# Kernel tuning notes

Measured on AMD Instinct MI355X. Metric: run time of the kernel, lower is better.

Reference implementation:

```python
import jax, jax.numpy as jnp
import numpy as np

N = 50000      # n_nodes
E = 800000     # n_edges
IN_NF = 64     # in_node_nf
HID = 128      # hidden_nf
OUT_NF = 64    # out_node_nf
L = 4          # n_layers
EH = HID // 2  # edge MLP hidden width (edge_nf_ratio=2)
C = 1.0        # aggregation scaling constant


def _w(k, shape):
    # fan-in scaled init (matches nn.Linear scale roughly)
    return jax.random.normal(k, shape, dtype=jnp.float32) / np.sqrt(shape[-2]).astype(np.float32)


def setup_inputs() -> dict:
    key = jax.random.key(0)
    ks = jax.random.split(key, 10)
    h = jax.random.normal(ks[0], (N, IN_NF), dtype=jnp.float32)
    edges = jax.random.randint(ks[1], (2, E), 0, N, dtype=jnp.int32)
    return {
        "h": h,
        "edges": edges,
        "W_in": _w(ks[2], (IN_NF, HID)),
        "b_in": jnp.zeros((HID,), jnp.float32),
        # stacked per-layer GCL params, leading dim L
        "eW1": _w(ks[3], (L, 2 * HID, EH)),
        "eb1": jnp.zeros((L, EH), jnp.float32),
        "eW2": _w(ks[4], (L, EH, EH)),
        "eb2": jnp.zeros((L, EH), jnp.float32),
        "nW1": _w(ks[5], (L, HID + EH, HID)),
        "nb1": jnp.zeros((L, HID), jnp.float32),
        "nW2": _w(ks[6], (L, HID, HID)),
        "nb2": jnp.zeros((L, HID), jnp.float32),
        "W_out": _w(ks[7], (HID, OUT_NF)),
        "b_out": jnp.zeros((OUT_NF,), jnp.float32),
    }


def reference(h, edges, W_in, b_in, eW1, eb1, eW2, eb2, nW1, nb1, nW2, nb2, W_out, b_out):
    row, col = edges[0], edges[1]
    h = h @ W_in + b_in  # [N, HID] embedding_in

    def layer(hc, p):
        w1, b1, w2, b2, m1, c1, m2, c2 = p
        # edge model: gather endpoints, concat, 2-layer SiLU MLP
        m = jnp.concatenate([hc[row], hc[col]], axis=1)          # [E, 2*HID]
        m = jax.nn.silu(m @ w1 + b1)                             # [E, EH]
        m = jax.nn.silu(m @ w2 + b2)                             # [E, EH]
        # node model: scatter-sum messages to source nodes, scale by C
        agg = jax.ops.segment_sum(m, row, num_segments=N) * C    # [N, EH]
        z = jnp.concatenate([hc, agg], axis=1)                   # [N, HID+EH]
        z = jax.nn.silu(z @ m1 + c1)
        z = z @ m2 + c2                                          # [N, HID]
        return hc + z, None  # residual=True

    h, _ = jax.lax.scan(layer, h, (eW1, eb1, eW2, eb2, nW1, nb1, nW2, nb2))
    return h @ W_out + b_out  # [N, OUT_NF] embedding_out
```

## Files before the change

### kernel.cpp

```cpp
#include <hip/hip_runtime.h>
#include <hip/hip_bf16.h>
#include <hip/hip_fp16.h>
#include <cstdint>
#include <cstddef>

#define N_NODES 50000
#define N_EDGES 800000
#define NBKT    196
#define BSH     8
#define BCHUNK  2048
#define CAP     6144

typedef __attribute__((ext_vector_type(8))) short short8;
typedef __attribute__((ext_vector_type(4))) float floatx4;
typedef __attribute__((ext_vector_type(2))) float floatx2;
typedef __attribute__((ext_vector_type(4))) unsigned int uintx4;
typedef __attribute__((ext_vector_type(2))) unsigned int uintx2;
typedef __attribute__((ext_vector_type(8))) _Float16 half8v;

__device__ inline float bf2f(unsigned short u) {
    union { unsigned int i; float f; } v; v.i = ((unsigned int)u) << 16; return v.f;
}
__device__ inline unsigned short f2bf(float f) {
    union { float f; unsigned int i; } v; v.f = f;
    unsigned int u = v.i;
    return (unsigned short)((u + 0x7FFFu + ((u >> 16) & 1u)) >> 16);
}
__device__ inline unsigned int f2bf_pk(float a, float b) {
    __hip_bfloat162 h2 = __float22bfloat162_rn(make_float2(a, b));
    return *reinterpret_cast<unsigned int*>(&h2);
}
__device__ inline unsigned short f2fh(float f) {
    _Float16 h = (_Float16)f;
    return __builtin_bit_cast(unsigned short, h);
}
__device__ inline unsigned int f2fh_pk(float a, float b) {
    typedef __attribute__((ext_vector_type(2))) __fp16 h2v;
    h2v r = __builtin_amdgcn_cvt_pkrtz(a, b);
    return __builtin_bit_cast(unsigned int, r);
}
__device__ inline __half2 u2h(unsigned int u) { return __builtin_bit_cast(__half2, u); }
__device__ inline unsigned int h2u(__half2 h) { return __builtin_bit_cast(unsigned int, h); }
__device__ inline __half2 silu_h2(__half2 x) {
    const __half2 nlog2e = __float2half2_rn(-1.4426950408889634f);
    const __half2 one    = __float2half2_rn(1.0f);
    __half2 e = h2exp2(__hmul2(x, nlog2e));
    return __hmul2(x, h2rcp(__hadd2(e, one)));
}
__device__ inline float silu_f(float x) {
    float e = __expf(-x);
    return x * __builtin_amdgcn_rcpf(1.0f + e);
}

__device__ inline int block_excl_scan_256(int v, int* buf) {
    int tid = threadIdx.x;
    buf[tid] = v;
    __syncthreads();
    #pragma unroll
    for (int off = 1; off < 256; off <<= 1) {
        int t = (tid >= off) ? buf[tid - off] : 0;
        __syncthreads();
        buf[tid] += t;
        __syncthreads();
    }
    return buf[tid] - v;
}

__device__ inline void pack_std(const float* __restrict__ src,
                                unsigned short* __restrict__ dst,
                                int NOUT, long j) {
    int i = (int)(j & 7);
    long rest = j >> 3;
    int n = (int)(rest % NOUT);
    int kb = (int)(rest / NOUT);
    dst[j] = f2bf(src[(long)(kb * 8 + i) * NOUT + n]);
}
__device__ inline void pack_std_h(const float* __restrict__ src,
                                  unsigned short* __restrict__ dst,
                                  int NOUT, long j) {
    int i = (int)(j & 7);
    long rest = j >> 3;
    int n = (int)(rest % NOUT);
    int kb = (int)(rest / NOUT);
    dst[j] = f2fh(src[(long)(kb * 8 + i) * NOUT + n]);
}

#define SW_IN 8192L
#define SW_OUT 8192L
#define SW1   16384L
#define SE2   4096L
#define SN1   24576L
#define SN2   16384L
#define SB    128L
#define PERL  (SW1 + SE2 + SN1 + SN2 + SB)
#define PACK_TOTAL (SW_IN + SW_OUT + 4 * PERL)
#define PACK_GRID_TOTAL (PACK_TOTAL + NBKT)

__global__ __launch_bounds__(256) void pack_kernel(
    const float* __restrict__ W_in,
    const float* __restrict__ W_out, const float* __restrict__ eW1,
    const float* __restrict__ eb1, const float* __restrict__ eW2,
    const float* __restrict__ nW1, const float* __restrict__ nW2,
    unsigned short* __restrict__ Winp,
    unsigned short* __restrict__ Woutp, unsigned short* __restrict__ W1p,
    unsigned short* __restrict__ eW2p, unsigned short* __restrict__ nW1p,
    unsigned short* __restrict__ nW2p, float* __restrict__ biasP,
    int* __restrict__ countB)
{
    long idx = (long)blockIdx.x * 256 + threadIdx.x;
    if (idx >= PACK_TOTAL) {
        long t = idx - PACK_TOTAL;
        if (t < NBKT) countB[t] = 0;
        return;
    }
    long j = idx;
    if (j < SW_IN) { pack_std(W_in, Winp, 128, j); return; }
    j -= SW_IN;
    if (j < SW_OUT) { pack_std(W_out, Woutp, 64, j); return; }
    j -= SW_OUT;
    int l = (int)(j / PERL);
    long r = j % PERL;
    if (r < SW1) {
        int i = (int)(r & 7);
        int n = (int)((r >> 3) & 127);
        int kb = (int)(r >> 10);
        int k = kb * 8 + i;
        const float* w = eW1 + (long)l * 256 * 64;
        float v = (n < 64) ? w[(long)k * 64 + n] : w[(long)(128 + k) * 64 + (n - 64)];
        W1p[(long)l * SW1 + r] = f2bf(v);
        return;
    }
    r -= SW1;
    if (r < SE2) { pack_std_h(eW2 + (long)l * 4096, eW2p + (long)l * SE2, 64, r); return; }
    r -= SE2;
    if (r < SN1) { pack_std(nW1 + (long)l * 24576, nW1p + (long)l * SN1, 128, r); return; }
    r -= SN1;
    if (r < SN2) { pack_std(nW2 + (long)l * 16384, nW2p + (long)l * SN2, 128, r); return; }
    r -= SN2;
    biasP[(long)l * 128 + r] = (r < 64) ? eb1[(long)l * 64 + r] : 0.0f;
}

__global__ __launch_bounds__(256) void hist_k(const int* __restrict__ erow,
                                              int* __restrict__ countB, int E) {
    __shared__ int c[NBKT];
    for (int i = threadIdx.x; i < NBKT; i += 256) c[i] = 0;
    __syncthreads();
    int j = blockIdx.x * BCHUNK + threadIdx.x;
    #pragma unroll
    for (int i = 0; i < BCHUNK / 256; i++, j += 256)
        if (j < E) atomicAdd(&c[erow[j] >> BSH], 1);
    __syncthreads();
    for (int i = threadIdx.x; i < NBKT; i += 256)
        if (c[i]) atomicAdd(&countB[i], c[i]);
}

__global__ __launch_bounds__(256) void bucket_scan_k(const int* __restrict__ countB,
                                                     int* __restrict__ bucketBase,
                                                     int* __restrict__ bucketCursor) {
    __shared__ int buf[256];
    int tid = threadIdx.x;
    int v = (tid < NBKT) ? countB[tid] : 0;
    int excl = block_excl_scan_256(v, buf);
    if (tid < NBKT) {
        bucketBase[tid] = excl;
        bucketCursor[tid] = excl;
    }
    if (tid == NBKT - 1) bucketBase[NBKT] = excl + v;
}

__global__ __launch_bounds__(256) void bin_k(
    const int* __restrict__ erow, const int* __restrict__ ecol,
    int* __restrict__ bucketCursor, int2* __restrict__ binned, int E)
{
    __shared__ int2 staged[BCHUNK];
    __shared__ int cnt[NBKT];
    __shared__ int binStart[NBKT];
    __shared__ int gbase[NBKT];
    __shared__ int scanbuf[256];
    const int tid = threadIdx.x;
    const int base = blockIdx.x * BCHUNK;
    const int nloc = min(BCHUNK, E - base);

    for (int i = tid; i < NBKT; i += 256) cnt[i] = 0;
    __syncthreads();

    int2 ed[BCHUNK / 256];
    int  bo[BCHUNK / 256];
    #pragma unroll
    for (int i = 0; i < BCHUNK / 256; i++) {
        int jl = i * 256 + tid;
        if (jl < nloc) {
            int j = base + jl;
            int r = erow[j], c = ecol[j];
            ed[i] = make_int2(r, c);
            int b = r >> BSH;
            int off = atomicAdd(&cnt[b], 1);
            bo[i] = (b << 12) | off;
        } else bo[i] = -1;
    }
    __syncthreads();

    int v = (tid < NBKT) ? cnt[tid] : 0;
    int excl = block_excl_scan_256(v, scanbuf);
    if (tid < NBKT) binStart[tid] = excl;
    if (tid < NBKT && v > 0) gbase[tid] = atomicAdd(&bucketCursor[tid], v);
    __syncthreads();

    #pragma unroll
    for (int i = 0; i < BCHUNK / 256; i++) {
        if (bo[i] >= 0)
            staged[binStart[bo[i] >> 12] + (bo[i] & 0xFFF)] = ed[i];
    }
    __syncthreads();

    for (int j = tid; j < nloc; j += 256) {
        int2 e = staged[j];
        int b = e.x >> BSH;
        binned[gbase[b] + (j - binStart[b])] = e;
    }
}

__global__ __launch_bounds__(256) void sort_k(
    const int2* __restrict__ binned, const int* __restrict__ bucketBase,
    int2* __restrict__ eidx)
{
    __shared__ int2 st[CAP];
    __shared__ int cnt[256];
    __shared__ int cur[256];
    __shared__ int scanbuf[256];
    const int b = blockIdx.x;
    const int tid = threadIdx.x;
    const int s0 = bucketBase[b];
    int n = bucketBase[b + 1] - s0;
    if (n > CAP) n = CAP;

    cnt[tid] = 0;
    __syncthreads();
    for (int j = tid; j < n; j += 256) {
        int2 e = binned[s0 + j];
        st[j] = e;
        atomicAdd(&cnt[e.x & 255], 1);
    }
    __syncthreads();
    int excl = block_excl_scan_256(cnt[tid], scanbuf);
    cur[tid] = excl;
    __syncthreads();
    for (int j = tid; j < n; j += 256) {
        int2 e = st[j];
        int pos = atomicAdd(&cur[e.x & 255], 1);
        eidx[s0 + pos] = e;
    }
}

__global__ __launch_bounds__(256) void edge_fused_k(
    const int2* __restrict__ eidx,
    const unsigned short* __restrict__ P,
    const unsigned short* __restrict__ Bp,
    const float* __restrict__ b2, float* __restrict__ agg, int E)
{
    __shared__ float M2s[64 * 68];
    __shared__ int ridS[64];
    __shared__ short segStartS[66];
    __shared__ int nsegS;
    const int tid = threadIdx.x;
    const int wave = tid >> 6;
    const int lane = tid & 63;
    const int lrow = lane & 15;
    const int quad = lane >> 4;
    const int e0 = blockIdx.x * 64;
    const int el = wave * 16 + lrow;
    const int e = e0 + el;

    floatx4 acc[4];
    #pragma unroll
    for (int nt = 0; nt < 4; nt++) {
        float bv = b2[nt * 16 + lrow];
        acc[nt] = (floatx4){bv, bv, bv, bv};
    }

    half8v af0 = {};
    half8v af1 = {};
    if (e < E) {
        int2 rc = eidx[e];
        int rr = rc.x, cc = rc.y;
        if (quad == 0) ridS[el] = rr;
        const uintx4* pt = (const uintx4*)(P + (size_t)rr * 128 + quad * 8);
        const uintx4* pb = (const uintx4*)(P + (size_t)cc * 128 + 64 + quad * 8);
        uintx4 t0 = pt[0], t1 = pt[4];
        uintx4 b0 = pb[0], b1 = pb[4];
        uintx4 O0, O1;
        #pragma unroll
        for (int i = 0; i < 4; i++) {
            O0[i] = h2u(silu_h2(__hadd2(u2h(t0[i]), u2h(b0[i]))));
            O1[i] = h2u(silu_h2(__hadd2(u2h(t1[i]), u2h(b1[i]))));
        }
        af0 = __builtin_bit_cast(half8v, O0);
        af1 = __builtin_bit_cast(half8v, O1);
    } else if (quad == 0) {
        ridS[el] = -1;
    }

    #pragma unroll
    for (int nt = 0; nt < 4; nt++) {
        half8v bf0 = *(const half8v*)(Bp + (size_t)((0 * 4 + quad) * 64 + nt * 16 + lrow) * 8);
        acc[nt] = __builtin_amdgcn_mfma_f32_16x16x32_f16(af0, bf0, acc[nt], 0, 0, 0);
        half8v bf1 = *(const half8v*)(Bp + (size_t)((1 * 4 + quad) * 64 + nt * 16 + lrow) * 8);
        acc[nt] = __builtin_amdgcn_mfma_f32_16x16x32_f16(af1, bf1, acc[nt], 0, 0, 0);
    }

    #pragma unroll
    for (int nt = 0; nt < 4; nt++) {
        int n = nt * 16 + lrow;
        #pragma unroll
        for (int r = 0; r < 4; r++) {
            int el2 = wave * 16 + quad * 4 + r;
            M2s[el2 * 68 + n] = silu_f(acc[nt][r]);
        }
    }
    __syncthreads();

    if (tid < 64) {
        bool st = (ridS[tid] >= 0) && (tid == 0 || ridS[tid] != ridS[tid - 1]);
        unsigned long long m = __ballot(st);
        if (st) {
            int pos = __popcll(m & ((1ull << tid) - 1));
            segStartS[pos] = (short)tid;
        }
        if (tid == 0) {
            int ns = __popcll(m);
            nsegS = ns;
            int nvalid = E - e0;
            if (nvalid > 64) nvalid = 64;
            segStartS[ns] = (short)nvalid;
        }
    }
    __syncthreads();

    {
        int f = tid & 63;
        int g = tid >> 6;
        int ns = nsegS;
        for (int j = g; j < ns; j += 4) {
            int a = segStartS[j], b = segStartS[j + 1];
            float s = 0.0f;
            for (int el2 = a; el2 < b; el2++) s += M2s[el2 * 68 + f];
            int rv = ridS[a];
            if (j == 0 || j == ns - 1)
                atomicAdd(&agg[(size_t)rv * 64 + f], s);
            else
                agg[(size_t)rv * 64 + f] = s;
        }
    }
}

#define SROW 264
template<int FINAL>
__global__ __launch_bounds__(512) void node_fused_k(
    const unsigned short* __restrict__ hbf, const float* __restrict__ agg,
    const unsigned short* __restrict__ W1, const float* __restrict__ b1,
    const unsigned short* __restrict__ W2, const float* __restrict__ b2,
    const unsigned short* __restrict__ B3, const float* __restrict__ bias3,
    unsigned short* __restrict__ hB, unsigned short* __restrict__ Pout,
    float* __restrict__ outF, float* __restrict__ aggZ, int M)
{
    __shared__ unsigned short S[64 * SROW];
    const int tid = threadIdx.x;
    const int m0 = blockIdx.x * 64;
    const int wave = tid >> 6;
    const int lane = tid & 63;
    const int lrow = lane & 15;
    const int quad = lane >> 4;
    const int g = wave >> 1;
    const int h = wave & 1;
    const int elb = g * 16 + quad * 4;

    short8 afa0, afa1;
    {
        const float* ap = agg + (size_t)(m0 + g * 16 + lrow) * 64;
        floatx4 q0 = *(const floatx4*)(ap + quad * 8);
        floatx4 q1 = *(const floatx4*)(ap + quad * 8 + 4);
        floatx4 q2 = *(const floatx4*)(ap + 32 + quad * 8);
        floatx4 q3 = *(const floatx4*)(ap + 32 + quad * 8 + 4);
        unsigned int c0[4] = { f2bf_pk(q0[0], q0[1]), f2bf_pk(q0[2], q0[3]),
                               f2bf_pk(q1[0], q1[1]), f2bf_pk(q1[2], q1[3]) };
        unsigned int c1[4] = { f2bf_pk(q2[0], q2[1]), f2bf_pk(q2[2], q2[3]),
                               f2bf_pk(q3[0], q3[1]), f2bf_pk(q3[2], q3[3]) };
        afa0 = *(const short8*)c0;
        afa1 = *(const short8*)c1;
    }

    for (int t = tid; t < 64 * 16; t += 512) {
        int rr = t >> 4, c = t & 15;
        int row = m0 + rr;
        uintx4 val = {0, 0, 0, 0};
        if (row < M) val = *(const uintx4*)(hbf + (size_t)row * 128 + c * 8);
        *(uintx4*)(&S[rr * SROW + c * 8]) = val;
    }
    __syncthreads();

    if (!FINAL) {
        floatx4 z = {0, 0, 0, 0};
        for (int t = tid; t < 64 * 16; t += 512) {
            int rr = t >> 4, c = t & 15;
            int row = m0 + rr;
            if (row < M) *(floatx4*)(aggZ + (size_t)row * 64 + c * 4) = z;
        }
    }

    const unsigned short* arow = &S[(g * 16 + lrow) * SROW];

    floatx4 acc[4];
    #pragma unroll
    for (int i = 0; i < 4; i++) acc[i] = (floatx4){0, 0, 0, 0};
    #pragma unroll
    for (int kt = 0; kt < 4; kt++) {
        short8 afrag = *(const short8*)(arow + kt * 32 + quad * 8);
        int kb = kt * 4 + quad;
        #pragma unroll
        for (int j = 0; j < 4; j++) {
            int n = (4 * h + j) * 16 + lrow;
            short8 bfrag = *(const short8*)(W1 + (size_t)(kb * 128 + n) * 8);
            acc[j] = __builtin_amdgcn_mfma_f32_16x16x32_bf16(afrag, bfrag, acc[j], 0, 0, 0);
        }
    }
    #pragma unroll
    for (int j = 0; j < 4; j++) {
        int n = (4 * h + j) * 16 + lrow;
        short8 b4 = *(const short8*)(W1 + (size_t)((16 + quad) * 128 + n) * 8);
        acc[j] = __builtin_amdgcn_mfma_f32_16x16x32_bf16(afa0, b4, acc[j], 0, 0, 0);
        short8 b5 = *(const short8*)(W1 + (size_t)((20 + quad) * 128 + n) * 8);
        acc[j] = __builtin_amdgcn_mfma_f32_16x16x32_bf16(afa1, b5, acc[j], 0, 0, 0);
    }

    #pragma unroll
    for (int j = 0; j < 4; j++) {
        int n = (4 * h + j) * 16 + lrow;
        float bv = b1[n];
        unsigned int p01 = f2bf_pk(silu_f(acc[j][0] + bv), silu_f(acc[j][1] + bv));
        unsigned int p23 = f2bf_pk(silu_f(acc[j][2] + bv), silu_f(acc[j][3] + bv));
        S[(elb + 0) * SROW + 128 + n] = (unsigned short)(p01 & 0xFFFF);
        S[(elb + 1) * SROW + 128 + n] = (unsigned short)(p01 >> 16);
        S[(elb + 2) * SROW + 128 + n] = (unsigned short)(p23 & 0xFFFF);
        S[(elb + 3) * SROW + 128 + n] = (unsigned short)(p23 >> 16);
    }
    __syncthreads();

    floatx4 acc2[4];
    #pragma unroll
    for (int i = 0; i < 4; i++) acc2[i] = (floatx4){0, 0, 0, 0};
    #pragma unroll
    for (int kt = 0; kt < 4; kt++) {
        short8 afrag = *(const short8*)(arow + 128 + kt * 32 + quad * 8);
        int kb = kt * 4 + quad;
        #pragma unroll
        for (int j = 0; j < 4; j++) {
            int n = (4 * h + j) * 16 + lrow;
            short8 bfrag = *(const short8*)(W2 + (size_t)(kb * 128 + n) * 8);
            acc2[j] = __builtin_amdgcn_mfma_f32_16x16x32_bf16(afrag, bfrag, acc2[j], 0, 0, 0);
        }
    }

    #pragma unroll
    for (int j = 0; j < 4; j++) {
        int n = (4 * h + j) * 16 + lrow;
        float bv = b2[n];
        floatx4 v4;
        #pragma unroll
        for (int r = 0; r < 4; r++) {
            float res = bf2f(S[(elb + r) * SROW + n]);
            v4[r] = acc2[j][r] + bv + res;
        }
        unsigned int p01 = f2bf_pk(v4[0], v4[1]);
        unsigned int p23 = f2bf_pk(v4[2], v4[3]);
        S[(elb + 0) * SROW + n] = (unsigned short)(p01 & 0xFFFF);
        S[(elb + 1) * SROW + n] = (unsigned short)(p01 >> 16);
        S[(elb + 2) * SROW + n] = (unsigned short)(p23 & 0xFFFF);
        S[(elb + 3) * SROW + n] = (unsigned short)(p23 >> 16);
    }
    __syncthreads();

    constexpr int NT3 = FINAL ? 2 : 4;
    constexpr int NO3 = FINAL ? 64 : 128;
    floatx4 acc3[NT3];
    #pragma unroll
    for (int i = 0; i < NT3; i++) acc3[i] = (floatx4){0, 0, 0, 0};
    #pragma unroll
    for (int kt = 0; kt < 4; kt++) {
        short8 afrag = *(const short8*)(arow + kt * 32 + quad * 8);
        int kb = kt * 4 + quad;
        #pragma unroll
        for (int j = 0; j < NT3; j++) {
            int n = (NT3 * h + j) * 16 + lrow;
            short8 bfrag = *(const short8*)(B3 + (size_t)(kb * NO3 + n) * 8);
            acc3[j] = __builtin_amdgcn_mfma_f32_16x16x32_bf16(afrag, bfrag, acc3[j], 0, 0, 0);
        }
    }
    #pragma unroll
    for (int j = 0; j < NT3; j++) {
        int n = (NT3 * h + j) * 16 + lrow;
        float bv = bias3[n];
        if (FINAL) {
            #pragma unroll
            for (int r = 0; r < 4; r++)
                ((float*)(&S[(elb + r) * SROW + 128]))[n] = acc3[j][r] + bv;
        } else {
            unsigned int p01 = f2fh_pk(acc3[j][0] + bv, acc3[j][1] + bv);
            unsigned int p23 = f2fh_pk(acc3[j][2] + bv, acc3[j][3] + bv);
            S[(elb + 0) * SROW + 128 + n] = (unsigned short)(p01 & 0xFFFF);
            S[(elb + 1) * SROW + 128 + n] = (unsigned short)(p01 >> 16);
            S[(elb + 2) * SROW + 128 + n] = (unsigned short)(p23 & 0xFFFF);
            S[(elb + 3) * SROW + 128 + n] = (unsigned short)(p23 >> 16);
        }
    }
    __syncthreads();

    if (FINAL) {
        for (int t = tid; t < 64 * 16; t += 512) {
            int rr = t >> 4, c = t & 15;
            int row = m0 + rr;
            if (row < M)
                *(floatx4*)(outF + (size_t)row * 64 + c * 4) =
                    *(const floatx4*)((const float*)(&S[rr * SROW + 128]) + c * 4);
        }
    } else {
        for (int t = tid; t < 64 * 32; t += 512) {
            int rr = t >> 5, c = t & 31;
            int row = m0 + rr;
            if (row < M) {
                if (c < 16)
                    *(uintx4*)(hB + (size_t)row * 128 + c * 8) =
                        *(const uintx4*)(&S[rr * SROW + c * 8]);
                else
                    *(uintx4*)(Pout + (size_t)row * 128 + (c - 16) * 8) =
                        *(const uintx4*)(&S[rr * SROW + 128 + (c - 16) * 8]);
            }
        }
    }
}

#define SROWE 264
__global__ __launch_bounds__(256) void embed_fused_k(
    const float* __restrict__ h0, const unsigned short* __restrict__ Win,
    const float* __restrict__ b_in, const unsigned short* __restrict__ W1,
    const float* __restrict__ biasP,
    unsigned short* __restrict__ hB, unsigned short* __restrict__ Pout,
    float* __restrict__ aggZ, int M)
{
    __shared__ unsigned short S[64 * SROWE];
    const int tid = threadIdx.x;
    const int m0 = blockIdx.x * 64;
    const int wave = tid >> 6;
    const int lane = tid & 63;
    const int lrow = lane & 15;
    const int quad = lane >> 4;
    const int elb = wave * 16 + quad * 4;

    for (int t = tid; t < 64 * 16; t += 256) {
        int rr = t >> 4, c = t & 15;
        int row = m0 + rr;
        floatx4 v = {0, 0, 0, 0};
        if (row < M) v = *(const floatx4*)(h0 + (size_t)row * 64 + c * 4);
        uintx2 u = { f2bf_pk(v[0], v[1]), f2bf_pk(v[2], v[3]) };
        *(uintx2*)(&S[rr * SROWE + c * 4]) = u;
    }
    __syncthreads();

    {
        floatx4 z = {0, 0, 0, 0};
        for (int t = tid; t < 64 * 16; t += 256) {
            int rr = t >> 4, c = t & 15;
            int row = m0 + rr;
            if (row < M) *(floatx4*)(aggZ + (size_t)row * 64 + c * 4) = z;
        }
    }

    const unsigned short* arow = &S[(wave * 16 + lrow) * SROWE];

    floatx4 acc[8];
    #pragma unroll
    for (int i = 0; i < 8; i++) acc[i] = (floatx4){0, 0, 0, 0};
    #pragma unroll
    for (int kt = 0; kt < 2; kt++) {
        short8 afrag = *(const short8*)(arow + kt * 32 + quad * 8);
        int kb = kt * 4 + quad;
        #pragma unroll
        for (int nt = 0; nt < 8; nt++) {
            short8 bfrag = *(const short8*)(Win + (size_t)(kb * 128 + nt * 16 + lrow) * 8);
            acc[nt] = __builtin_amdgcn_mfma_f32_16x16x32_bf16(afrag, bfrag, acc[nt], 0, 0, 0);
        }
    }

    #pragma unroll
    for (int nt = 0; nt < 8; nt++) {
        int n = nt * 16 + lrow;
        float bv = b_in[n];
        floatx4 v4;
        #pragma unroll
        for (int r = 0; r < 4; r++) v4[r] = acc[nt][r] + bv;
        unsigned int p01 = f2bf_pk(v4[0], v4[1]);
        unsigned int p23 = f2bf_pk(v4[2], v4[3]);
        S[(elb + 0) * SROWE + n] = (unsigned short)(p01 & 0xFFFF);
        S[(elb + 1) * SROWE + n] = (unsigned short)(p01 >> 16);
        S[(elb + 2) * SROWE + n] = (unsigned short)(p23 & 0xFFFF);
        S[(elb + 3) * SROWE + n] = (unsigned short)(p23 >> 16);
    }

    floatx4 acc3[8];
    #pragma unroll
    for (int i = 0; i < 8; i++) acc3[i] = (floatx4){0, 0, 0, 0};
    #pragma unroll
    for (int kt = 0; kt < 4; kt++) {
        short8 afrag = *(const short8*)(arow + kt * 32 + quad * 8);
        int kb = kt * 4 + quad;
        #pragma unroll
        for (int nt = 0; nt < 8; nt++) {
            short8 bfrag = *(const short8*)(W1 + (size_t)(kb * 128 + nt * 16 + lrow) * 8);
            acc3[nt] = __builtin_amdgcn_mfma_f32_16x16x32_bf16(afrag, bfrag, acc3[nt], 0, 0, 0);
        }
    }
    #pragma unroll
    for (int nt = 0; nt < 8; nt++) {
        int n = nt * 16 + lrow;
        float bv = biasP[n];
        unsigned int p01 = f2fh_pk(acc3[nt][0] + bv, acc3[nt][1] + bv);
        unsigned int p23 = f2fh_pk(acc3[nt][2] + bv, acc3[nt][3] + bv);
        S[(elb + 0) * SROWE + 128 + n] = (unsigned short)(p01 & 0xFFFF);
        S[(elb + 1) * SROWE + 128 + n] = (unsigned short)(p01 >> 16);
        S[(elb + 2) * SROWE + 128 + n] = (unsigned short)(p23 & 0xFFFF);
        S[(elb + 3) * SROWE + 128 + n] = (unsigned short)(p23 >> 16);
    }
    __syncthreads();

    for (int t = tid; t < 64 * 32; t += 256) {
        int rr = t / 32, c = t % 32;
        int row = m0 + rr;
        if (row < M) {
            if (c < 16)
                *(uintx4*)(hB + (size_t)row * 128 + c * 8) =
                    *(const uintx4*)(&S[rr * SROWE + c * 8]);
            else
                *(uintx4*)(Pout + (size_t)row * 128 + (c - 16) * 8) =
                    *(const uintx4*)(&S[rr * SROWE + 128 + (c - 16) * 8]);
        }
    }
}

extern "C" void kernel_launch(void* const* d_in, const int* in_sizes, int n_in,
                              void* d_out, int out_size, void* d_ws, size_t ws_size,
                              hipStream_t stream) {
    const float* h0   = (const float*)d_in[0];
    const int*   edges= (const int*)d_in[1];
    const float* W_in = (const float*)d_in[2];
    const float* b_in = (const float*)d_in[3];
    const float* eW1  = (const float*)d_in[4];
    const float* eb1  = (const float*)d_in[5];
    const float* eW2  = (const float*)d_in[6];
    const float* eb2  = (const float*)d_in[7];
    const float* nW1  = (const float*)d_in[8];
    const float* nb1  = (const float*)d_in[9];
    const float* nW2  = (const float*)d_in[10];
    const float* nb2  = (const float*)d_in[11];
    const float* W_out= (const float*)d_in[12];
    const float* b_out= (const float*)d_in[13];
    float* out = (float*)d_out;

    const int E = in_sizes[1] / 2;
    const int* erow = edges;
    const int* ecol = edges + E;

    char* ws = (char*)d_ws;
    unsigned short* hbf  = (unsigned short*)(ws + 0);
    unsigned short* P    = (unsigned short*)(ws + 38424576);
    float*          agg  = (float*)(ws + 51224576);
    int2*           binned=(int2*)(ws + 51224576);
    int2*           eidx = (int2*)(ws + 76824576);
    float*          biasP= (float*)(ws + 83224576);
    unsigned short* Winp = (unsigned short*)(ws + 83226624);
    unsigned short* Woutp= (unsigned short*)(ws + 83243008);
    unsigned short* W1p  = (unsigned short*)(ws + 83259392);
    unsigned short* eW2p = (unsigned short*)(ws + 83390464);
    unsigned short* nW1p = (unsigned short*)(ws + 83423232);
    unsigned short* nW2p = (unsigned short*)(ws + 83619840);
    int*            countB=(int*)(ws + 83750912);
    int*            bucketBase=(int*)(ws + 83751936);
    int*            bucketCursor=(int*)(ws + 83752960);

    const int gemm_grid = (N_NODES + 63) / 64;
    const int edge_grid = (E + 63) / 64;
    const int pack_grid = (int)((PACK_GRID_TOTAL + 255) / 256);
    const int bin_grid  = (E + BCHUNK - 1) / BCHUNK;

    pack_kernel<<<pack_grid, 256, 0, stream>>>(W_in, W_out, eW1, eb1, eW2,
                                               nW1, nW2, Winp, Woutp, W1p,
                                               eW2p, nW1p, nW2p, biasP, countB);

    hist_k<<<bin_grid, 256, 0, stream>>>(erow, countB, E);
    bucket_scan_k<<<1, 256, 0, stream>>>(countB, bucketBase, bucketCursor);
    bin_k<<<bin_grid, 256, 0, stream>>>(erow, ecol, bucketCursor, binned, E);
    sort_k<<<NBKT, 256, 0, stream>>>(binned, bucketBase, eidx);

    embed_fused_k<<<gemm_grid, 256, 0, stream>>>(
        h0, Winp, b_in, W1p, biasP, hbf, P, agg, N_NODES);

    for (int l = 0; l < 4; l++) {
        edge_fused_k<<<edge_grid, 256, 0, stream>>>(
            eidx, P, eW2p + (size_t)l * SE2, eb2 + (size_t)l * 64, agg, E);
        if (l < 3) {
            node_fused_k<0><<<gemm_grid, 512, 0, stream>>>(
                hbf, agg, nW1p + (size_t)l * SN1, nb1 + (size_t)l * 128,
                nW2p + (size_t)l * SN2, nb2 + (size_t)l * 128,
                W1p + (size_t)(l + 1) * SW1, biasP + (size_t)(l + 1) * 128,
                hbf, P, nullptr, agg, N_NODES);
        } else {
            node_fused_k<1><<<gemm_grid, 512, 0, stream>>>(
                hbf, agg, nW1p + (size_t)l * SN1, nb1 + (size_t)l * 128,
                nW2p + (size_t)l * SN2, nb2 + (size_t)l * 128,
                Woutp, b_out, nullptr, nullptr, out, nullptr, N_NODES);
        }
    }
}
```

Measured before the change: 401.1 us.

## Merge bucket scan and embedding into binning kernel to cut launches

Drops the single-block bucket scan kernel. Each binning block and each sort block now recomputes the 196-entry exclusive scan of bucket counts, and cursors start at zero in the pack kernel. The binning work and the embedding GEMM run as different block ranges of one launch, so they can overlap and two launches are saved. The binned buffer moves to its own workspace region so it no longer overlaps agg, which the embedding blocks zero in the same launch.

```diff
diff --git a/kernel.cpp b/kernel.cpp
--- a/kernel.cpp
+++ b/kernel.cpp
@@ -94,7 +94,7 @@
 #define SB    128L
 #define PERL  (SW1 + SE2 + SN1 + SN2 + SB)
 #define PACK_TOTAL (SW_IN + SW_OUT + 4 * PERL)
-#define PACK_GRID_TOTAL (PACK_TOTAL + NBKT)
+#define PACK_GRID_TOTAL (PACK_TOTAL + 2 * NBKT)
 
 __global__ __launch_bounds__(256) void pack_kernel(
     const float* __restrict__ W_in,
@@ -105,12 +105,13 @@
     unsigned short* __restrict__ Woutp, unsigned short* __restrict__ W1p,
     unsigned short* __restrict__ eW2p, unsigned short* __restrict__ nW1p,
     unsigned short* __restrict__ nW2p, float* __restrict__ biasP,
-    int* __restrict__ countB)
+    int* __restrict__ countB, int* __restrict__ bucketCursor)
 {
     long idx = (long)blockIdx.x * 256 + threadIdx.x;
     if (idx >= PACK_TOTAL) {
         long t = idx - PACK_TOTAL;
         if (t < NBKT) countB[t] = 0;
+        else if (t < 2 * NBKT) bucketCursor[t - NBKT] = 0;
         return;
     }
     long j = idx;
@@ -154,84 +155,194 @@
         if (c[i]) atomicAdd(&countB[i], c[i]);
 }
 
-__global__ __launch_bounds__(256) void bucket_scan_k(const int* __restrict__ countB,
-                                                     int* __restrict__ bucketBase,
-                                                     int* __restrict__ bucketCursor) {
-    __shared__ int buf[256];
-    int tid = threadIdx.x;
-    int v = (tid < NBKT) ? countB[tid] : 0;
-    int excl = block_excl_scan_256(v, buf);
-    if (tid < NBKT) {
-        bucketBase[tid] = excl;
-        bucketCursor[tid] = excl;
-    }
-    if (tid == NBKT - 1) bucketBase[NBKT] = excl + v;
-}
-
-__global__ __launch_bounds__(256) void bin_k(
+#define SROWE 264
+#define BE_SMEM_BYTES (64 * SROWE * 2)
+
+__global__ __launch_bounds__(256) void bin_embed_k(
     const int* __restrict__ erow, const int* __restrict__ ecol,
-    int* __restrict__ bucketCursor, int2* __restrict__ binned, int E)
+    const int* __restrict__ countB, int* __restrict__ bucketCursor,
+    int2* __restrict__ binned, int E, int binGrid,
+    const float* __restrict__ h0, const unsigned short* __restrict__ Win,
+    const float* __restrict__ b_in, const unsigned short* __restrict__ W1,
+    const float* __restrict__ biasP,
+    unsigned short* __restrict__ hB, unsigned short* __restrict__ Pout,
+    float* __restrict__ aggZ, int M)
 {
-    __shared__ int2 staged[BCHUNK];
-    __shared__ int cnt[NBKT];
-    __shared__ int binStart[NBKT];
-    __shared__ int gbase[NBKT];
-    __shared__ int scanbuf[256];
+    __shared__ char SMEM[BE_SMEM_BYTES];
     const int tid = threadIdx.x;
-    const int base = blockIdx.x * BCHUNK;
-    const int nloc = min(BCHUNK, E - base);
-
-    for (int i = tid; i < NBKT; i += 256) cnt[i] = 0;
-    __syncthreads();
-
-    int2 ed[BCHUNK / 256];
-    int  bo[BCHUNK / 256];
-    #pragma unroll
-    for (int i = 0; i < BCHUNK / 256; i++) {
-        int jl = i * 256 + tid;
-        if (jl < nloc) {
-            int j = base + jl;
-            int r = erow[j], c = ecol[j];
-            ed[i] = make_int2(r, c);
-            int b = r >> BSH;
-            int off = atomicAdd(&cnt[b], 1);
-            bo[i] = (b << 12) | off;
-        } else bo[i] = -1;
-    }
-    __syncthreads();
-
-    int v = (tid < NBKT) ? cnt[tid] : 0;
-    int excl = block_excl_scan_256(v, scanbuf);
-    if (tid < NBKT) binStart[tid] = excl;
-    if (tid < NBKT && v > 0) gbase[tid] = atomicAdd(&bucketCursor[tid], v);
-    __syncthreads();
-
-    #pragma unroll
-    for (int i = 0; i < BCHUNK / 256; i++) {
-        if (bo[i] >= 0)
-            staged[binStart[bo[i] >> 12] + (bo[i] & 0xFFF)] = ed[i];
-    }
-    __syncthreads();
-
-    for (int j = tid; j < nloc; j += 256) {
-        int2 e = staged[j];
-        int b = e.x >> BSH;
-        binned[gbase[b] + (j - binStart[b])] = e;
+
+    if (blockIdx.x < binGrid) {
+        int* cnt      = (int*)SMEM;
+        int* binStart = cnt + NBKT;
+        int* gbase    = binStart + NBKT;
+        int* scanbuf  = gbase + NBKT;
+        int2* staged  = (int2*)(scanbuf + 256);
+
+        const int base = blockIdx.x * BCHUNK;
+        const int nloc = min(BCHUNK, E - base);
+
+        int vcb = (tid < NBKT) ? countB[tid] : 0;
+        int exclB = block_excl_scan_256(vcb, scanbuf);
+
+        for (int i = tid; i < NBKT; i += 256) cnt[i] = 0;
+        __syncthreads();
+
+        int2 ed[BCHUNK / 256];
+        int  bo[BCHUNK / 256];
+        #pragma unroll
+        for (int i = 0; i < BCHUNK / 256; i++) {
+            int jl = i * 256 + tid;
+            if (jl < nloc) {
+                int j = base + jl;
+                int r = erow[j], c = ecol[j];
+                ed[i] = make_int2(r, c);
+                int b = r >> BSH;
+                int off = atomicAdd(&cnt[b], 1);
+                bo[i] = (b << 12) | off;
+            } else bo[i] = -1;
+        }
+        __syncthreads();
+
+        int v = (tid < NBKT) ? cnt[tid] : 0;
+        int excl = block_excl_scan_256(v, scanbuf);
+        if (tid < NBKT) binStart[tid] = excl;
+        if (tid < NBKT && v > 0)
+            gbase[tid] = exclB + atomicAdd(&bucketCursor[tid], v);
+        __syncthreads();
+
+        #pragma unroll
+        for (int i = 0; i < BCHUNK / 256; i++) {
+            if (bo[i] >= 0)
+                staged[binStart[bo[i] >> 12] + (bo[i] & 0xFFF)] = ed[i];
+        }
+        __syncthreads();
+
+        for (int j = tid; j < nloc; j += 256) {
+            int2 e = staged[j];
+            int b = e.x >> BSH;
+            binned[gbase[b] + (j - binStart[b])] = e;
+        }
+        return;
+    }
+
+    unsigned short* S = (unsigned short*)SMEM;
+    const int m0 = (blockIdx.x - binGrid) * 64;
+    const int wave = tid >> 6;
+    const int lane = tid & 63;
+    const int lrow = lane & 15;
+    const int quad = lane >> 4;
+    const int elb = wave * 16 + quad * 4;
+
+    for (int t = tid; t < 64 * 16; t += 256) {
+        int rr = t >> 4, c = t & 15;
+        int row = m0 + rr;
+        floatx4 v = {0, 0, 0, 0};
+        if (row < M) v = *(const floatx4*)(h0 + (size_t)row * 64 + c * 4);
+        uintx2 u = { f2bf_pk(v[0], v[1]), f2bf_pk(v[2], v[3]) };
+        *(uintx2*)(&S[rr * SROWE + c * 4]) = u;
+    }
+    __syncthreads();
+
+    {
+        floatx4 z = {0, 0, 0, 0};
+        for (int t = tid; t < 64 * 16; t += 256) {
+            int rr = t >> 4, c = t & 15;
+            int row = m0 + rr;
+            if (row < M) *(floatx4*)(aggZ + (size_t)row * 64 + c * 4) = z;
+        }
+    }
+
+    const unsigned short* arow = &S[(wave * 16 + lrow) * SROWE];
+
+    floatx4 acc[8];
+    #pragma unroll
+    for (int i = 0; i < 8; i++) acc[i] = (floatx4){0, 0, 0, 0};
+    #pragma unroll
+    for (int kt = 0; kt < 2; kt++) {
+        short8 afrag = *(const short8*)(arow + kt * 32 + quad * 8);
+        int kb = kt * 4 + quad;
+        #pragma unroll
+        for (int nt = 0; nt < 8; nt++) {
+            short8 bfrag = *(const short8*)(Win + (size_t)(kb * 128 + nt * 16 + lrow) * 8);
+            acc[nt] = __builtin_amdgcn_mfma_f32_16x16x32_bf16(afrag, bfrag, acc[nt], 0, 0, 0);
+        }
+    }
+
+    #pragma unroll
+    for (int nt = 0; nt < 8; nt++) {
+        int n = nt * 16 + lrow;
+        float bv = b_in[n];
+        floatx4 v4;
+        #pragma unroll
+        for (int r = 0; r < 4; r++) v4[r] = acc[nt][r] + bv;
+        unsigned int p01 = f2bf_pk(v4[0], v4[1]);
+        unsigned int p23 = f2bf_pk(v4[2], v4[3]);
+        S[(elb + 0) * SROWE + n] = (unsigned short)(p01 & 0xFFFF);
+        S[(elb + 1) * SROWE + n] = (unsigned short)(p01 >> 16);
+        S[(elb + 2) * SROWE + n] = (unsigned short)(p23 & 0xFFFF);
+        S[(elb + 3) * SROWE + n] = (unsigned short)(p23 >> 16);
+    }
+
+    floatx4 acc3[8];
+    #pragma unroll
+    for (int i = 0; i < 8; i++) acc3[i] = (floatx4){0, 0, 0, 0};
+    #pragma unroll
+    for (int kt = 0; kt < 4; kt++) {
+        short8 afrag = *(const short8*)(arow + kt * 32 + quad * 8);
+        int kb = kt * 4 + quad;
+        #pragma unroll
+        for (int nt = 0; nt < 8; nt++) {
+            short8 bfrag = *(const short8*)(W1 + (size_t)(kb * 128 + nt * 16 + lrow) * 8);
+            acc3[nt] = __builtin_amdgcn_mfma_f32_16x16x32_bf16(afrag, bfrag, acc3[nt], 0, 0, 0);
+        }
+    }
+    #pragma unroll
+    for (int nt = 0; nt < 8; nt++) {
+        int n = nt * 16 + lrow;
+        float bv = biasP[n];
+        unsigned int p01 = f2fh_pk(acc3[nt][0] + bv, acc3[nt][1] + bv);
+        unsigned int p23 = f2fh_pk(acc3[nt][2] + bv, acc3[nt][3] + bv);
+        S[(elb + 0) * SROWE + 128 + n] = (unsigned short)(p01 & 0xFFFF);
+        S[(elb + 1) * SROWE + 128 + n] = (unsigned short)(p01 >> 16);
+        S[(elb + 2) * SROWE + 128 + n] = (unsigned short)(p23 & 0xFFFF);
+        S[(elb + 3) * SROWE + 128 + n] = (unsigned short)(p23 >> 16);
+    }
+    __syncthreads();
+
+    for (int t = tid; t < 64 * 32; t += 256) {
+        int rr = t / 32, c = t % 32;
+        int row = m0 + rr;
+        if (row < M) {
+            if (c < 16)
+                *(uintx4*)(hB + (size_t)row * 128 + c * 8) =
+                    *(const uintx4*)(&S[rr * SROWE + c * 8]);
+            else
+                *(uintx4*)(Pout + (size_t)row * 128 + (c - 16) * 8) =
+                    *(const uintx4*)(&S[rr * SROWE + 128 + (c - 16) * 8]);
+        }
     }
 }
 
 __global__ __launch_bounds__(256) void sort_k(
-    const int2* __restrict__ binned, const int* __restrict__ bucketBase,
+    const int2* __restrict__ binned, const int* __restrict__ countB,
     int2* __restrict__ eidx)
 {
     __shared__ int2 st[CAP];
     __shared__ int cnt[256];
     __shared__ int cur[256];
     __shared__ int scanbuf[256];
+    __shared__ int baseS[2];
     const int b = blockIdx.x;
     const int tid = threadIdx.x;
-    const int s0 = bucketBase[b];
-    int n = bucketBase[b + 1] - s0;
+
+    {
+        int v = (tid < NBKT) ? countB[tid] : 0;
+        int excl = block_excl_scan_256(v, scanbuf);
+        if (tid == b) { baseS[0] = excl; baseS[1] = excl + v; }
+    }
+    __syncthreads();
+    const int s0 = baseS[0];
+    int n = baseS[1] - s0;
     if (n > CAP) n = CAP;
 
     cnt[tid] = 0;
@@ -538,113 +649,6 @@
     }
 }
 
-#define SROWE 264
-__global__ __launch_bounds__(256) void embed_fused_k(
-    const float* __restrict__ h0, const unsigned short* __restrict__ Win,
-    const float* __restrict__ b_in, const unsigned short* __restrict__ W1,
-    const float* __restrict__ biasP,
-    unsigned short* __restrict__ hB, unsigned short* __restrict__ Pout,
-    float* __restrict__ aggZ, int M)
-{
-    __shared__ unsigned short S[64 * SROWE];
-    const int tid = threadIdx.x;
-    const int m0 = blockIdx.x * 64;
-    const int wave = tid >> 6;
-    const int lane = tid & 63;
-    const int lrow = lane & 15;
-    const int quad = lane >> 4;
-    const int elb = wave * 16 + quad * 4;
-
-    for (int t = tid; t < 64 * 16; t += 256) {
-        int rr = t >> 4, c = t & 15;
-        int row = m0 + rr;
-        floatx4 v = {0, 0, 0, 0};
-        if (row < M) v = *(const floatx4*)(h0 + (size_t)row * 64 + c * 4);
-        uintx2 u = { f2bf_pk(v[0], v[1]), f2bf_pk(v[2], v[3]) };
-        *(uintx2*)(&S[rr * SROWE + c * 4]) = u;
-    }
-    __syncthreads();
-
-    {
-        floatx4 z = {0, 0, 0, 0};
-        for (int t = tid; t < 64 * 16; t += 256) {
-            int rr = t >> 4, c = t & 15;
-            int row = m0 + rr;
-            if (row < M) *(floatx4*)(aggZ + (size_t)row * 64 + c * 4) = z;
-        }
-    }
-
-    const unsigned short* arow = &S[(wave * 16 + lrow) * SROWE];
-
-    floatx4 acc[8];
-    #pragma unroll
-    for (int i = 0; i < 8; i++) acc[i] = (floatx4){0, 0, 0, 0};
-    #pragma unroll
-    for (int kt = 0; kt < 2; kt++) {
-        short8 afrag = *(const short8*)(arow + kt * 32 + quad * 8);
-        int kb = kt * 4 + quad;
-        #pragma unroll
-        for (int nt = 0; nt < 8; nt++) {
-            short8 bfrag = *(const short8*)(Win + (size_t)(kb * 128 + nt * 16 + lrow) * 8);
-            acc[nt] = __builtin_amdgcn_mfma_f32_16x16x32_bf16(afrag, bfrag, acc[nt], 0, 0, 0);
-        }
-    }
-
-    #pragma unroll
-    for (int nt = 0; nt < 8; nt++) {
-        int n = nt * 16 + lrow;
-        float bv = b_in[n];
-        floatx4 v4;
-        #pragma unroll
-        for (int r = 0; r < 4; r++) v4[r] = acc[nt][r] + bv;
-        unsigned int p01 = f2bf_pk(v4[0], v4[1]);
-        unsigned int p23 = f2bf_pk(v4[2], v4[3]);
-        S[(elb + 0) * SROWE + n] = (unsigned short)(p01 & 0xFFFF);
-        S[(elb + 1) * SROWE + n] = (unsigned short)(p01 >> 16);
-        S[(elb + 2) * SROWE + n] = (unsigned short)(p23 & 0xFFFF);
-        S[(elb + 3) * SROWE + n] = (unsigned short)(p23 >> 16);
-    }
-
-    floatx4 acc3[8];
-    #pragma unroll
-    for (int i = 0; i < 8; i++) acc3[i] = (floatx4){0, 0, 0, 0};
-    #pragma unroll
-    for (int kt = 0; kt < 4; kt++) {
-        short8 afrag = *(const short8*)(arow + kt * 32 + quad * 8);
-        int kb = kt * 4 + quad;
-        #pragma unroll
-        for (int nt = 0; nt < 8; nt++) {
-            short8 bfrag = *(const short8*)(W1 + (size_t)(kb * 128 + nt * 16 + lrow) * 8);
-            acc3[nt] = __builtin_amdgcn_mfma_f32_16x16x32_bf16(afrag, bfrag, acc3[nt], 0, 0, 0);
-        }
-    }
-    #pragma unroll
-    for (int nt = 0; nt < 8; nt++) {
-        int n = nt * 16 + lrow;
-        float bv = biasP[n];
-        unsigned int p01 = f2fh_pk(acc3[nt][0] + bv, acc3[nt][1] + bv);
-        unsigned int p23 = f2fh_pk(acc3[nt][2] + bv, acc3[nt][3] + bv);
-        S[(elb + 0) * SROWE + 128 + n] = (unsigned short)(p01 & 0xFFFF);
-        S[(elb + 1) * SROWE + 128 + n] = (unsigned short)(p01 >> 16);
-        S[(elb + 2) * SROWE + 128 + n] = (unsigned short)(p23 & 0xFFFF);
-        S[(elb + 3) * SROWE + 128 + n] = (unsigned short)(p23 >> 16);
-    }
-    __syncthreads();
-
-    for (int t = tid; t < 64 * 32; t += 256) {
-        int rr = t / 32, c = t % 32;
-        int row = m0 + rr;
-        if (row < M) {
-            if (c < 16)
-                *(uintx4*)(hB + (size_t)row * 128 + c * 8) =
-                    *(const uintx4*)(&S[rr * SROWE + c * 8]);
-            else
-                *(uintx4*)(Pout + (size_t)row * 128 + (c - 16) * 8) =
-                    *(const uintx4*)(&S[rr * SROWE + 128 + (c - 16) * 8]);
-        }
-    }
-}
-
 extern "C" void kernel_launch(void* const* d_in, const int* in_sizes, int n_in,
                               void* d_out, int out_size, void* d_ws, size_t ws_size,
                               hipStream_t stream) {
@@ -670,9 +674,9 @@
 
     char* ws = (char*)d_ws;
     unsigned short* hbf  = (unsigned short*)(ws + 0);
+    int2*           binned=(int2*)(ws + 12800000);
     unsigned short* P    = (unsigned short*)(ws + 38424576);
     float*          agg  = (float*)(ws + 51224576);
-    int2*           binned=(int2*)(ws + 51224576);
     int2*           eidx = (int2*)(ws + 76824576);
     float*          biasP= (float*)(ws + 83224576);
     unsigned short* Winp = (unsigned short*)(ws + 83226624);
@@ -682,7 +686,6 @@
     unsigned short* nW1p = (unsigned short*)(ws + 83423232);
     unsigned short* nW2p = (unsigned short*)(ws + 83619840);
     int*            countB=(int*)(ws + 83750912);
-    int*            bucketBase=(int*)(ws + 83751936);
     int*            bucketCursor=(int*)(ws + 83752960);
 
     const int gemm_grid = (N_NODES + 63) / 64;
@@ -692,15 +695,16 @@
 
     pack_kernel<<<pack_grid, 256, 0, stream>>>(W_in, W_out, eW1, eb1, eW2,
                                                nW1, nW2, Winp, Woutp, W1p,
-                                               eW2p, nW1p, nW2p, biasP, countB);
+                                               eW2p, nW1p, nW2p, biasP,
+                                               countB, bucketCursor);
 
     hist_k<<<bin_grid, 256, 0, stream>>>(erow, countB, E);
-    bucket_scan_k<<<1, 256, 0, stream>>>(countB, bucketBase, bucketCursor);
-    bin_k<<<bin_grid, 256, 0, stream>>>(erow, ecol, bucketCursor, binned, E);
-    sort_k<<<NBKT, 256, 0, stream>>>(binned, bucketBase, eidx);
-
-    embed_fused_k<<<gemm_grid, 256, 0, stream>>>(
+
+    bin_embed_k<<<bin_grid + gemm_grid, 256, 0, stream>>>(
+        erow, ecol, countB, bucketCursor, binned, E, bin_grid,
         h0, Winp, b_in, W1p, biasP, hbf, P, agg, N_NODES);
+
+    sort_k<<<NBKT, 256, 0, stream>>>(binned, countB, eidx);
 
     for (int l = 0; l < 4; l++) {
         edge_fused_k<<<edge_grid, 256, 0, stream>>>(
```

New measurement: 396.9 us. About the same (-1.0%).
